# Kernel tuning notes

Hardware: AMD Instinct MI355X
Metric: run time of the kernel (lower is better)

## Reference

```python
import jax, jax.numpy as jnp
import numpy as np

B, CIN, COUT, K, E, H, W = 32, 128, 256, 3, 8, 64, 64


def setup_inputs() -> dict:
    key = jax.random.key(0)
    k1, k2, k3, k4 = jax.random.split(key, 4)
    x = jax.random.normal(k1, (B, CIN, H, W), dtype=jnp.float32)
    expert_weight = jax.random.normal(k2, (E, COUT, CIN, K, K), dtype=jnp.float32)
    # nn.Linear(in_channels, num_experts): weight [E, CIN], bias [E]
    bound = 1.0 / np.sqrt(CIN)
    routing_w = jax.random.uniform(k3, (E, CIN), minval=-bound, maxval=bound, dtype=jnp.float32)
    routing_b = jax.random.uniform(k4, (E,), minval=-bound, maxval=bound, dtype=jnp.float32)
    return {"x": x, "expert_weight": expert_weight, "routing_w": routing_w, "routing_b": routing_b}


def reference(x, expert_weight, routing_w, routing_b):
    # routing: global-avg-pool -> linear -> softmax over experts
    pooled = x.mean(axis=(2, 3))                             # [B, CIN]
    logits = pooled @ routing_w.T + routing_b                # [B, E]
    rweights = jax.nn.softmax(logits, axis=-1)               # [B, E]
    # per-sample combined conv weights: [B, COUT, CIN, K, K]
    cw = jnp.einsum('be,eoikl->boikl', rweights, expert_weight)

    def conv_one(xi, wi):
        # xi: [CIN, H, W], wi: [COUT, CIN, K, K]; VALID conv, stride 1
        return jax.lax.conv_general_dilated(
            xi[None], wi, window_strides=(1, 1), padding='VALID',
            dimension_numbers=('NCHW', 'OIHW', 'NCHW'))[0]

    return jax.vmap(conv_one)(x, cw)                         # [B, COUT, H-K+1, W-K+1]
```

## Files before the change

### kernel.cpp

```cpp
#include <hip/hip_runtime.h>
#include <hip/hip_bf16.h>


#define CC_B    32
#define CC_CIN  128
#define CC_COUT 256
#define CC_NP   3844
#define CC_NT   18

typedef __attribute__((ext_vector_type(8))) short bf16x8;
typedef __attribute__((ext_vector_type(4))) float f32x4;

__global__ void cc_nhwc(const float* __restrict__ x, __hip_bfloat16* __restrict__ xn,
                        float* __restrict__ psum) {
    const int b = blockIdx.x >> 6, y = blockIdx.x & 63;
    __shared__ float lds[64 * 129];
    __shared__ float sred[256];
    const int t = threadIdx.x;
    const float* src = x + (size_t)b * CC_CIN * 4096 + y * 64;
#pragma unroll
    for (int i = 0; i < 32; ++i) {
        const int idx = i * 256 + t;
        const int cin = idx >> 6, xx = idx & 63;
        lds[xx * 129 + cin] = src[(size_t)cin * 4096 + xx];
    }
    __syncthreads();
    __hip_bfloat16* dst = xn + ((size_t)b * 4096 + y * 64) * CC_CIN;
#pragma unroll
    for (int j = 0; j < 4; ++j) {
        const int cidx = j * 256 + t;
        const int xx = cidx >> 4, c8 = (cidx & 15) * 8;
        union { __hip_bfloat16 h[8]; uint4 v; } u;
#pragma unroll
        for (int jj = 0; jj < 8; ++jj) u.h[jj] = __float2bfloat16(lds[xx * 129 + c8 + jj]);
        *reinterpret_cast<uint4*>(dst + (size_t)xx * CC_CIN + c8) = u.v;
    }
    const int cin = t & 127, xh = (t >> 7) * 32;
    float s = 0.f;
#pragma unroll
    for (int xx = 0; xx < 32; ++xx) s += lds[(xh + xx) * 129 + cin];
    sred[t] = s;
    __syncthreads();
    if (t < 128) psum[((size_t)b * 64 + y) * CC_CIN + t] = sred[t] + sred[t + 128];
}

__global__ void cc_reduce(const float* __restrict__ psum, float* __restrict__ pooled) {
    const int b = blockIdx.x, c = threadIdx.x;
    const float* p = psum + (size_t)b * 64 * CC_CIN + c;
    float s = 0.f;
#pragma unroll 8
    for (int y = 0; y < 64; ++y) s += p[(size_t)y * CC_CIN];
    pooled[b * CC_CIN + c] = s * (1.f / 4096.f);
}

__global__ void cc_routing(const float* __restrict__ pooled,
                           const float* __restrict__ rw_w,
                           const float* __restrict__ rw_b,
                           float* __restrict__ rweights) {
    const int t = threadIdx.x;
    const int b = t >> 3, e = t & 7;
    const float* p = pooled + b * CC_CIN;
    const float* w = rw_w + e * CC_CIN;
    float acc = rw_b[e];
#pragma unroll 8
    for (int i = 0; i < CC_CIN; ++i) acc += p[i] * w[i];
    float m = acc;
#pragma unroll
    for (int off = 1; off < 8; off <<= 1) m = fmaxf(m, __shfl_xor(m, off, 64));
    const float ex = __expf(acc - m);
    float sum = ex;
#pragma unroll
    for (int off = 1; off < 8; off <<= 1) sum += __shfl_xor(sum, off, 64);
    rweights[t] = ex / sum;
}

__global__ void cc_combine(const float* __restrict__ ew,
                           const float* __restrict__ rw,
                           __hip_bfloat16* __restrict__ cw) {
    const int t9 = blockIdx.x >> 8;
    const int cout = blockIdx.x & 255;
    const int cin = threadIdx.x;
    __shared__ float rws[256];
    rws[cin] = rw[cin];
    rws[cin + 128] = rw[cin + 128];
    __syncthreads();
    float wv[8];
    const size_t base = ((size_t)cout * CC_CIN + cin) * 9 + t9;
#pragma unroll
    for (int e = 0; e < 8; ++e) wv[e] = ew[base + (size_t)e * (CC_COUT * CC_CIN * 9)];
#pragma unroll 4
    for (int b = 0; b < CC_B; ++b) {
        float acc = 0.f;
#pragma unroll
        for (int e = 0; e < 8; ++e) acc += rws[b * 8 + e] * wv[e];
        cw[(((size_t)b * 9 + t9) * CC_COUT + cout) * CC_CIN + cin] = __float2bfloat16(acc);
    }
}

__device__ __forceinline__ void gload_lds16(const void* g, void* l) {
    __builtin_amdgcn_global_load_lds(
        (const __attribute__((address_space(1))) unsigned int*)g,
        (__attribute__((address_space(3))) unsigned int*)l, 16, 0, 0);
}

__global__ __launch_bounds__(256, 2) void cc_conv(
    const __hip_bfloat16* __restrict__ xn,
    const __hip_bfloat16* __restrict__ cw,
    float* __restrict__ out)
{
    __shared__ __align__(16) char smem[65536];
    const int l   = blockIdx.x;
    const int xcd = l & 7, li = l >> 3;
    const int b   = 4 * xcd + li / 62;
    const int r2  = li % 62;
    const int m0  = (r2 & 1) * 128;
    const int n0  = (r2 >> 1) * 128;

    const int tid = threadIdx.x;
    const int wid = tid >> 6, lane = tid & 63;
    const int waveM = wid >> 1, waveN = wid & 1;

    f32x4 acc[4][4];
#pragma unroll
    for (int i = 0; i < 4; ++i)
#pragma unroll
        for (int j = 0; j < 4; ++j) acc[i][j] = (f32x4){0.f, 0.f, 0.f, 0.f};

    const int gsw = (lane & 7) ^ (lane >> 3);
    int laOff[4], lbOff[4];
#pragma unroll
    for (int i = 0; i < 4; ++i) {
        const int row = wid * 32 + i * 8 + (lane >> 3);
        laOff[i] = (m0 + row) * CC_CIN + gsw * 8;
        int p = n0 + row; if (p > CC_NP - 1) p = CC_NP - 1;
        const int oy = p / 62, ox = p - oy * 62;
        lbOff[i] = (oy * 64 + ox) * CC_CIN + gsw * 8;
    }

    const __hip_bfloat16* cwb = cw + (size_t)b * 9 * CC_COUT * CC_CIN;
    const __hip_bfloat16* xnb = xn + (size_t)b * 4096 * CC_CIN;

    auto stageK = [&](int t) {
        const int t9 = t >> 1;
        const int ky = (t9 * 11) >> 5;
        const int kx = t9 - ky * 3;
        const int aoff = t9 * (CC_COUT * CC_CIN) + (t & 1) * 64;
        const int boff = (ky * 64 + kx) * CC_CIN + (t & 1) * 64;
        char* Ab = smem + (t & 1) * 16384 + wid * 4096;
        char* Bb = smem + 32768 + (t & 1) * 16384 + wid * 4096;
#pragma unroll
        for (int i = 0; i < 4; ++i)
            gload_lds16(cwb + aoff + laOff[i], Ab + i * 1024);
#pragma unroll
        for (int i = 0; i < 4; ++i)
            gload_lds16(xnb + boff + lbOff[i], Bb + i * 1024);
    };

    const int rl = lane & 15, q = lane >> 4;

    stageK(0);
    stageK(1);

#pragma unroll 1
    for (int t = 0; t < CC_NT; ++t) {
        const char* Ab = smem + (t & 1) * 16384;
        const char* Bb = smem + 32768 + (t & 1) * 16384;

        if (t < CC_NT - 1) asm volatile("s_waitcnt vmcnt(8)" ::: "memory");
        else               asm volatile("s_waitcnt vmcnt(0)" ::: "memory");
        asm volatile("s_barrier" ::: "memory");

        bf16x8 af[8], bf[8];
#pragma unroll
        for (int mf = 0; mf < 4; ++mf)
#pragma unroll
            for (int kk = 0; kk < 2; ++kk) {
                const int r = waveM * 64 + mf * 16 + rl;
                af[mf * 2 + kk] = *(const bf16x8*)(Ab + r * 128 + (((kk * 4 + q) ^ (r & 7)) * 16));
            }
#pragma unroll
        for (int nf = 0; nf < 4; ++nf)
#pragma unroll
            for (int kk = 0; kk < 2; ++kk) {
                const int r = waveN * 64 + nf * 16 + rl;
                bf[nf * 2 + kk] = *(const bf16x8*)(Bb + r * 128 + (((kk * 4 + q) ^ (r & 7)) * 16));
            }
#pragma unroll
        for (int mf = 0; mf < 4; ++mf)
#pragma unroll
            for (int nf = 0; nf < 4; ++nf)
#pragma unroll
                for (int kk = 0; kk < 2; ++kk)
                    acc[mf][nf] = __builtin_amdgcn_mfma_f32_16x16x32_bf16(
                        af[mf * 2 + kk], bf[nf * 2 + kk], acc[mf][nf], 0, 0, 0);

        asm volatile("s_waitcnt lgkmcnt(0)" ::: "memory");
        asm volatile("s_barrier" ::: "memory");
        if (t + 2 < CC_NT) stageK(t + 2);
    }

    const int q4 = (lane >> 4) * 4;
#pragma unroll
    for (int mf = 0; mf < 4; ++mf) {
        const int crow = m0 + waveM * 64 + mf * 16 + q4;
#pragma unroll
        for (int nf = 0; nf < 4; ++nf) {
            const int p = n0 + waveN * 64 + nf * 16 + (lane & 15);
            if (p < CC_NP) {
                const size_t ob = ((size_t)b * CC_COUT + crow) * CC_NP + p;
#pragma unroll
                for (int j = 0; j < 4; ++j) out[ob + (size_t)j * CC_NP] = acc[mf][nf][j];
            }
        }
    }
}

extern "C" void kernel_launch(void* const* d_in, const int* in_sizes, int n_in,
                              void* d_out, int out_size, void* d_ws, size_t ws_size,
                              hipStream_t stream) {
    const float* x   = (const float*)d_in[0];
    const float* ew  = (const float*)d_in[1];
    const float* rww = (const float*)d_in[2];
    const float* rwb = (const float*)d_in[3];
    float* out = (float*)d_out;
    char* ws = (char*)d_ws;

    __hip_bfloat16* xnhwc = (__hip_bfloat16*)ws;
    __hip_bfloat16* cwcmb = (__hip_bfloat16*)(ws + 33554432);
    float* psum   = (float*)(ws + 52428800);
    float* pooled = (float*)(ws + 53477376);
    float* rwts   = (float*)(ws + 53493760);

    cc_nhwc<<<dim3(CC_B * 64), dim3(256), 0, stream>>>(x, xnhwc, psum);
    cc_reduce<<<dim3(CC_B), dim3(128), 0, stream>>>(psum, pooled);
    cc_routing<<<dim3(1), dim3(256), 0, stream>>>(pooled, rww, rwb, rwts);
    cc_combine<<<dim3(9 * CC_COUT), dim3(128), 0, stream>>>(ew, rwts, cwcmb);
    cc_conv<<<dim3(1984), dim3(256), 0, stream>>>(xnhwc, cwcmb, out);
}
```

Before: 127.2 us.

## Widen conv N-tile to 160, fuse routing kernels, reorder MFMA loop with setprio

The conv GEMM tile grows from 128x128 to 128x160 output pixels, giving 1600 blocks instead of 1984 and a larger B buffer in LDS (72KB). The aim is more reuse of A fragments and less tail waste across 3844 pixels. The pool-reduce and routing kernels are merged into one launch to save a launch. The K loop is fully unrolled, MFMAs are reordered kk-outer and wrapped in s_setprio, which adds register pressure with 20 accumulators and may reduce occupancy.

```diff
diff --git a/kernel.cpp b/kernel.cpp
--- a/kernel.cpp
+++ b/kernel.cpp
@@ -44,34 +44,37 @@
     if (t < 128) psum[((size_t)b * 64 + y) * CC_CIN + t] = sred[t] + sred[t + 128];
 }
 
-__global__ void cc_reduce(const float* __restrict__ psum, float* __restrict__ pooled) {
+__global__ void cc_route(const float* __restrict__ psum,
+                         const float* __restrict__ rw_w,
+                         const float* __restrict__ rw_b,
+                         float* __restrict__ rweights) {
     const int b = blockIdx.x, c = threadIdx.x;
+    __shared__ float pl[128];
+    __shared__ float lg[8];
     const float* p = psum + (size_t)b * 64 * CC_CIN + c;
     float s = 0.f;
 #pragma unroll 8
     for (int y = 0; y < 64; ++y) s += p[(size_t)y * CC_CIN];
-    pooled[b * CC_CIN + c] = s * (1.f / 4096.f);
-}
-
-__global__ void cc_routing(const float* __restrict__ pooled,
-                           const float* __restrict__ rw_w,
-                           const float* __restrict__ rw_b,
-                           float* __restrict__ rweights) {
-    const int t = threadIdx.x;
-    const int b = t >> 3, e = t & 7;
-    const float* p = pooled + b * CC_CIN;
-    const float* w = rw_w + e * CC_CIN;
-    float acc = rw_b[e];
+    pl[c] = s * (1.f / 4096.f);
+    __syncthreads();
+    if (c < 8) {
+        const float* w = rw_w + c * CC_CIN;
+        float a = rw_b[c];
 #pragma unroll 8
-    for (int i = 0; i < CC_CIN; ++i) acc += p[i] * w[i];
-    float m = acc;
-#pragma unroll
-    for (int off = 1; off < 8; off <<= 1) m = fmaxf(m, __shfl_xor(m, off, 64));
-    const float ex = __expf(acc - m);
-    float sum = ex;
-#pragma unroll
-    for (int off = 1; off < 8; off <<= 1) sum += __shfl_xor(sum, off, 64);
-    rweights[t] = ex / sum;
+        for (int i = 0; i < CC_CIN; ++i) a += pl[i] * w[i];
+        lg[c] = a;
+    }
+    __syncthreads();
+    if (c == 0) {
+        float m = lg[0];
+#pragma unroll
+        for (int e = 1; e < 8; ++e) m = fmaxf(m, lg[e]);
+        float ex[8], sm = 0.f;
+#pragma unroll
+        for (int e = 0; e < 8; ++e) { ex[e] = __expf(lg[e] - m); sm += ex[e]; }
+#pragma unroll
+        for (int e = 0; e < 8; ++e) rweights[b * 8 + e] = ex[e] / sm;
+    }
 }
 
 __global__ void cc_combine(const float* __restrict__ ew,
@@ -108,30 +111,35 @@
     const __hip_bfloat16* __restrict__ cw,
     float* __restrict__ out)
 {
-    __shared__ __align__(16) char smem[65536];
+    __shared__ __align__(16) char smem[73728];
     const int l   = blockIdx.x;
     const int xcd = l & 7, li = l >> 3;
-    const int b   = 4 * xcd + li / 62;
-    const int r2  = li % 62;
-    const int m0  = (r2 & 1) * 128;
-    const int n0  = (r2 >> 1) * 128;
+    const int b   = 4 * xcd + li / 50;
+    const int r2  = li % 50;
+    const int nt  = r2 >> 1, mt = r2 & 1;
+    const int m0  = mt * 128;
+    const int n0  = nt * 160;
 
     const int tid = threadIdx.x;
     const int wid = tid >> 6, lane = tid & 63;
     const int waveM = wid >> 1, waveN = wid & 1;
 
-    f32x4 acc[4][4];
+    f32x4 acc[4][5];
 #pragma unroll
     for (int i = 0; i < 4; ++i)
 #pragma unroll
-        for (int j = 0; j < 4; ++j) acc[i][j] = (f32x4){0.f, 0.f, 0.f, 0.f};
+        for (int j = 0; j < 5; ++j) acc[i][j] = (f32x4){0.f, 0.f, 0.f, 0.f};
 
     const int gsw = (lane & 7) ^ (lane >> 3);
-    int laOff[4], lbOff[4];
+    int laOff[4], lbOff[5];
 #pragma unroll
     for (int i = 0; i < 4; ++i) {
         const int row = wid * 32 + i * 8 + (lane >> 3);
         laOff[i] = (m0 + row) * CC_CIN + gsw * 8;
+    }
+#pragma unroll
+    for (int i = 0; i < 5; ++i) {
+        const int row = wid * 40 + i * 8 + (lane >> 3);
         int p = n0 + row; if (p > CC_NP - 1) p = CC_NP - 1;
         const int oy = p / 62, ox = p - oy * 62;
         lbOff[i] = (oy * 64 + ox) * CC_CIN + gsw * 8;
@@ -147,12 +155,12 @@
         const int aoff = t9 * (CC_COUT * CC_CIN) + (t & 1) * 64;
         const int boff = (ky * 64 + kx) * CC_CIN + (t & 1) * 64;
         char* Ab = smem + (t & 1) * 16384 + wid * 4096;
-        char* Bb = smem + 32768 + (t & 1) * 16384 + wid * 4096;
+        char* Bb = smem + 32768 + (t & 1) * 20480 + wid * 5120;
 #pragma unroll
         for (int i = 0; i < 4; ++i)
             gload_lds16(cwb + aoff + laOff[i], Ab + i * 1024);
 #pragma unroll
-        for (int i = 0; i < 4; ++i)
+        for (int i = 0; i < 5; ++i)
             gload_lds16(xnb + boff + lbOff[i], Bb + i * 1024);
     };
 
@@ -161,16 +169,16 @@
     stageK(0);
     stageK(1);
 
-#pragma unroll 1
+#pragma unroll
     for (int t = 0; t < CC_NT; ++t) {
         const char* Ab = smem + (t & 1) * 16384;
-        const char* Bb = smem + 32768 + (t & 1) * 16384;
-
-        if (t < CC_NT - 1) asm volatile("s_waitcnt vmcnt(8)" ::: "memory");
+        const char* Bb = smem + 32768 + (t & 1) * 20480;
+
+        if (t < CC_NT - 1) asm volatile("s_waitcnt vmcnt(9)" ::: "memory");
         else               asm volatile("s_waitcnt vmcnt(0)" ::: "memory");
         asm volatile("s_barrier" ::: "memory");
 
-        bf16x8 af[8], bf[8];
+        bf16x8 af[8], bf[10];
 #pragma unroll
         for (int mf = 0; mf < 4; ++mf)
 #pragma unroll
@@ -179,20 +187,22 @@
                 af[mf * 2 + kk] = *(const bf16x8*)(Ab + r * 128 + (((kk * 4 + q) ^ (r & 7)) * 16));
             }
 #pragma unroll
-        for (int nf = 0; nf < 4; ++nf)
+        for (int nf = 0; nf < 5; ++nf)
 #pragma unroll
             for (int kk = 0; kk < 2; ++kk) {
-                const int r = waveN * 64 + nf * 16 + rl;
+                const int r = waveN * 80 + nf * 16 + rl;
                 bf[nf * 2 + kk] = *(const bf16x8*)(Bb + r * 128 + (((kk * 4 + q) ^ (r & 7)) * 16));
             }
-#pragma unroll
-        for (int mf = 0; mf < 4; ++mf)
-#pragma unroll
-            for (int nf = 0; nf < 4; ++nf)
-#pragma unroll
-                for (int kk = 0; kk < 2; ++kk)
+        __builtin_amdgcn_s_setprio(1);
+#pragma unroll
+        for (int kk = 0; kk < 2; ++kk)
+#pragma unroll
+            for (int mf = 0; mf < 4; ++mf)
+#pragma unroll
+                for (int nf = 0; nf < 5; ++nf)
                     acc[mf][nf] = __builtin_amdgcn_mfma_f32_16x16x32_bf16(
                         af[mf * 2 + kk], bf[nf * 2 + kk], acc[mf][nf], 0, 0, 0);
+        __builtin_amdgcn_s_setprio(0);
 
         asm volatile("s_waitcnt lgkmcnt(0)" ::: "memory");
         asm volatile("s_barrier" ::: "memory");
@@ -204,8 +214,8 @@
     for (int mf = 0; mf < 4; ++mf) {
         const int crow = m0 + waveM * 64 + mf * 16 + q4;
 #pragma unroll
-        for (int nf = 0; nf < 4; ++nf) {
-            const int p = n0 + waveN * 64 + nf * 16 + (lane & 15);
+        for (int nf = 0; nf < 5; ++nf) {
+            const int p = n0 + waveN * 80 + nf * 16 + (lane & 15);
             if (p < CC_NP) {
                 const size_t ob = ((size_t)b * CC_COUT + crow) * CC_NP + p;
 #pragma unroll
@@ -228,12 +238,10 @@
     __hip_bfloat16* xnhwc = (__hip_bfloat16*)ws;
     __hip_bfloat16* cwcmb = (__hip_bfloat16*)(ws + 33554432);
     float* psum   = (float*)(ws + 52428800);
-    float* pooled = (float*)(ws + 53477376);
     float* rwts   = (float*)(ws + 53493760);
 
     cc_nhwc<<<dim3(CC_B * 64), dim3(256), 0, stream>>>(x, xnhwc, psum);
-    cc_reduce<<<dim3(CC_B), dim3(128), 0, stream>>>(psum, pooled);
-    cc_routing<<<dim3(1), dim3(256), 0, stream>>>(pooled, rww, rwb, rwts);
+    cc_route<<<dim3(CC_B), dim3(128), 0, stream>>>(psum, rww, rwb, rwts);
     cc_combine<<<dim3(9 * CC_COUT), dim3(128), 0, stream>>>(ew, rwts, cwcmb);
-    cc_conv<<<dim3(1984), dim3(256), 0, stream>>>(xnhwc, cwcmb, out);
-}
+    cc_conv<<<dim3(1600), dim3(256), 0, stream>>>(xnhwc, cwcmb, out);
+}
```

Result: faster. 124.4 us (-2.1%).
